# Kernel optimization log

Measured on AMD Instinct MI355X. Metric: run time of the kernel, lower is better.

The kernel has to match this reference:

```python
import jax, jax.numpy as jnp
import numpy as np

N_HEADS = 8
DIM_HEAD = 64


def _lin_params(key, fan_in, fan_out):
    k1, k2 = jax.random.split(key)
    w = jax.random.normal(k1, (fan_out, fan_in), jnp.float32) * 0.02
    b = jax.random.normal(k2, (fan_out,), jnp.float32) * 0.02
    return w, b


def setup_inputs() -> dict:
    key = jax.random.key(0)
    ks = jax.random.split(key, 16)
    n_nodes, n_edges = 30000, 480000
    input_nf, output_nf, hidden_nf = 128, 128, 256
    hd = N_HEADS * DIM_HEAD
    inp = {}
    inp['h'] = jax.random.normal(ks[0], (n_nodes, input_nf), jnp.float32)
    inp['x'] = jax.random.normal(ks[1], (n_nodes, 3), jnp.float32)
    inp['edge_index'] = jax.random.randint(ks[2], (2, n_edges), 0, n_nodes, jnp.int64)
    inp['mask'] = jnp.ones((n_edges,), jnp.bool_)
    inp['wq'], inp['bq'] = _lin_params(ks[3], input_nf, hd)
    inp['wk'], inp['bk'] = _lin_params(ks[4], input_nf, hd)
    inp['wv'], inp['bv'] = _lin_params(ks[5], input_nf, hd)
    inp['wo'], inp['bo'] = _lin_params(ks[6], hd, output_nf)
    inp['pw1'], inp['pb1'] = _lin_params(ks[7], 6, hidden_nf)
    inp['pw2'], inp['pb2'] = _lin_params(ks[8], hidden_nf, N_HEADS)
    inp['ew1'], inp['eb1'] = _lin_params(ks[9], 2 * input_nf + 7, hidden_nf)
    inp['ew2'], inp['eb2'] = _lin_params(ks[10], hidden_nf, hidden_nf)
    inp['eww'], inp['ewb'] = _lin_params(ks[11], hidden_nf, N_HEADS)
    inp['cw1'], inp['cb1'] = _lin_params(ks[12], 3, hidden_nf)
    inp['cw2'], inp['cb2'] = _lin_params(ks[13], hidden_nf, hidden_nf)
    inp['cw3'], inp['cb3'] = _lin_params(ks[14], hidden_nf, output_nf)
    return inp


def reference(h, x, edge_index, mask,
              wq, bq, wk, bk, wv, bv, wo, bo,
              pw1, pb1, pw2, pb2,
              ew1, eb1, ew2, eb2, eww, ewb,
              cw1, cb1, cw2, cb2, cw3, cb3):
    n_nodes = h.shape[0]
    row, col = edge_index[0], edge_index[1]
    # node projections -> [n, H, D]
    q = (h @ wq.T + bq).reshape(n_nodes, N_HEADS, DIM_HEAD)
    k = (h @ wk.T + bk).reshape(n_nodes, N_HEADS, DIM_HEAD)
    v = (h @ wv.T + bv).reshape(n_nodes, N_HEADS, DIM_HEAD)
    xr, xc = x[row], x[col]
    # pos encoding [E, H]
    abs_pos = jnp.concatenate([xr, xc], axis=-1)
    pos_enc = jax.nn.silu(abs_pos @ pw1.T + pb1) @ pw2.T + pb2
    # edge features -> per-head edge weights [E, H]
    rel_dist = jnp.sum((xr - xc) ** 2, axis=-1, keepdims=True)
    edge_attr = jnp.concatenate([h[row], h[col], rel_dist, xr, xc], axis=-1)
    edge_feat = jax.nn.silu(edge_attr @ ew1.T + eb1) @ ew2.T + eb2
    edge_w = edge_feat @ eww.T + ewb
    # attention scores [E, H]
    score = jnp.einsum('ehd,ehd->eh', q[row], k[col]) / (DIM_HEAD ** 0.5)
    score = score + pos_enc + edge_w
    score = jnp.where(mask[:, None], score, jnp.float32(-1e9))
    # scatter-softmax over edges grouped by destination (row)
    smax = jax.ops.segment_max(score, row, num_segments=n_nodes)
    escore = jnp.exp(score - smax[row])
    ssum = jax.ops.segment_sum(escore, row, num_segments=n_nodes)
    attn = escore / (ssum[row] + 1e-8)
    # weighted aggregation [n, H, D]
    agg = jax.ops.segment_sum(attn[:, :, None] * v[col], row, num_segments=n_nodes)
    out = agg.reshape(n_nodes, -1) @ wo.T + bo
    coord = jax.nn.silu(x @ cw1.T + cb1)
    coord = jax.nn.silu(coord @ cw2.T + cb2)
    coord = coord @ cw3.T + cb3
    return out + coord, jnp.zeros_like(x)
```

## Files before the change

kernel.cpp:

```cpp
#include <hip/hip_runtime.h>

typedef unsigned int uint;
typedef unsigned short ushort;
typedef unsigned char uchar;
typedef __attribute__((ext_vector_type(8))) short bf16x8;
typedef __attribute__((ext_vector_type(8))) ushort ushort8;
typedef __attribute__((ext_vector_type(4))) float f32x4;

__device__ __forceinline__ float silu_f(float t) { return t / (1.f + expf(-t)); }
__device__ __forceinline__ float silu_fast(float t) { return t / (1.f + __expf(-t)); }

__device__ __forceinline__ float bf2f(ushort u) {
  union { uint i; float f; } v; v.i = ((uint)u) << 16; return v.f;
}
__device__ __forceinline__ ushort f2bf(float f) {
  union { float f; uint i; } v; v.f = f;
  uint r = (v.i + 0x7fffu + ((v.i >> 16) & 1u)) >> 16;
  return (ushort)r;
}
__device__ __forceinline__ uchar f2e4m3(float f) {
  uint u = __float_as_uint(f);
  uint s = (u >> 24) & 0x80u;
  uint m = u & 0x7fffffffu;
  if (m >= 0x43f00000u) return (uchar)(s | 0x7e);
  if (m >= 0x3c800000u) {
    uint r = m + 0x7ffffu + ((m >> 20) & 1u);
    uint e = (r >> 23) - 120u;
    if (e > 15u) return (uchar)(s | 0x7e);
    return (uchar)(s | (e << 3) | ((r >> 20) & 7u));
  }
  float az = __uint_as_float(m);
  uint k = (uint)__float2int_rn(az * 512.f);
  return (uchar)(s | k);
}
__device__ __forceinline__ float e4m3f(uint b) {
  uint u = ((b & 0x80u) << 24) | ((b & 0x7fu) << 20);
  return __uint_as_float(u) * 0x1p+120f;
}

__global__ __launch_bounds__(256) void h2bf_kernel(const float* __restrict__ h,
                                                   ushort* __restrict__ h_bf, int total) {
  int idx = blockIdx.x * 256 + threadIdx.x;
  if (idx * 4 >= total) return;
  float4 v = *(const float4*)(h + idx * 4);
  ushort4 o;
  o.x = f2bf(v.x); o.y = f2bf(v.y); o.z = f2bf(v.z); o.w = f2bf(v.w);
  *(ushort4*)(h_bf + idx * 4) = o;
}

__global__ __launch_bounds__(256) void prep_wqkv(const float* __restrict__ wq,
                                                 const float* __restrict__ wk,
                                                 const float* __restrict__ wv,
                                                 const float* __restrict__ bq,
                                                 const float* __restrict__ bk,
                                                 const float* __restrict__ bv,
                                                 ushort* __restrict__ wqkv,
                                                 float* __restrict__ bqkv) {
  int idx = blockIdx.x * 256 + threadIdx.x;
  if (idx >= 1536 * 128) return;
  int j = idx >> 7, k = idx & 127;
  float v = (j < 512) ? wq[j * 128 + k]
          : (j < 1024) ? wk[(j - 512) * 128 + k]
          : wv[(j - 1024) * 128 + k];
  wqkv[idx] = f2bf(v);
  if (idx < 1536)
    bqkv[idx] = (idx < 512) ? bq[idx] : (idx < 1024) ? bk[idx - 512] : bv[idx - 1024];
}

__global__ __launch_bounds__(256) void prep_w1t(const float* __restrict__ ew1,
                                                const float* __restrict__ eb1,
                                                const float* __restrict__ pw1,
                                                const float* __restrict__ pb1,
                                                short* __restrict__ W1T,
                                                float* __restrict__ b1big) {
  int idx = blockIdx.x * 256 + threadIdx.x;
  if (idx >= 512 * 288) return;
  int n = idx / 288, k = idx % 288;
  float v = 0.f;
  if (n < 256) { if (k < 263) v = ew1[n * 263 + k]; }
  else         { if (k >= 257 && k < 263) v = pw1[(n - 256) * 6 + (k - 257)]; }
  W1T[idx] = (short)f2bf(v);
  if (idx < 512) b1big[idx] = (idx < 256) ? eb1[idx] : pb1[idx - 256];
}

__global__ __launch_bounds__(256) void prep_w2t(const float* __restrict__ ew2,
                                                const float* __restrict__ eww,
                                                const float* __restrict__ eb2,
                                                const float* __restrict__ ewb,
                                                const float* __restrict__ pw2,
                                                const float* __restrict__ pb2,
                                                short* __restrict__ W2T,
                                                float* __restrict__ biasC) {
  int idx = blockIdx.x * 256 + threadIdx.x;
  if (idx >= 16 * 512) return;
  int hh = idx >> 9, k = idx & 511;
  float v = 0.f;
  if (hh < 8) {
    if (k < 256) {
      float s = 0.f;
      for (int j = 0; j < 256; ++j) s += eww[hh * 256 + j] * ew2[j * 256 + k];
      v = s;
    } else {
      v = pw2[hh * 256 + (k - 256)];
    }
  }
  W2T[idx] = (short)f2bf(v);
  if (idx < 16) {
    float b = 0.f;
    if (idx < 8) {
      float s = 0.f;
      for (int j = 0; j < 256; ++j) s += eww[idx * 256 + j] * eb2[j];
      b = s + ewb[idx] + pb2[idx];
    }
    biasC[idx] = b;
  }
}

__global__ __launch_bounds__(256) void prep_wcomb(const float* __restrict__ wo,
                                                  const float* __restrict__ cw3,
                                                  const float* __restrict__ bo,
                                                  const float* __restrict__ cb3,
                                                  ushort* __restrict__ wcomb,
                                                  float* __restrict__ bcomb) {
  int idx = blockIdx.x * 256 + threadIdx.x;
  if (idx >= 128 * 768) return;
  int j = idx / 768, k = idx % 768;
  float v = (k < 512) ? wo[j * 512 + k] : cw3[j * 256 + (k - 512)];
  wcomb[idx] = f2bf(v);
  if (idx < 128) bcomb[idx] = bo[idx] + cb3[idx];
}

__global__ __launch_bounds__(256) void prep_cw2bf(const float* __restrict__ cw2,
                                                  ushort* __restrict__ cw2bf) {
  int idx = blockIdx.x * 256 + threadIdx.x;
  if (idx >= 256 * 256) return;
  cw2bf[idx] = f2bf(cw2[idx]);
}

__global__ __launch_bounds__(256) void qkv_mfma_kernel(
    const ushort* __restrict__ h_bf,
    const ushort* __restrict__ wqkv,
    const float* __restrict__ bqkv,
    ushort* __restrict__ q_t, uchar* __restrict__ k8, ushort* __restrict__ v_t,
    int n)
{
  __shared__ float oS[64 * 68];
  int tid = threadIdx.x;
  int lane = tid & 63, w = tid >> 6;
  int l15 = lane & 15, l4 = lane >> 4;
  int m0 = blockIdx.x * 64;
  int jb = blockIdx.y;
  int n0 = jb * 64 + w * 16;

  f32x4 acc[4];
#pragma unroll
  for (int mf = 0; mf < 4; ++mf) acc[mf] = (f32x4){0.f, 0.f, 0.f, 0.f};

#pragma unroll
  for (int ks = 0; ks < 4; ++ks) {
    bf16x8 bW = *(const bf16x8*)(wqkv + (size_t)(n0 + l15) * 128 + ks * 32 + l4 * 8);
#pragma unroll
    for (int mf = 0; mf < 4; ++mf) {
      int gr = m0 + mf * 16 + l15; if (gr >= n) gr = n - 1;
      bf16x8 aH = *(const bf16x8*)(h_bf + (size_t)gr * 128 + ks * 32 + l4 * 8);
      acc[mf] = __builtin_amdgcn_mfma_f32_16x16x32_bf16(aH, bW, acc[mf], 0, 0, 0);
    }
  }
#pragma unroll
  for (int mf = 0; mf < 4; ++mf)
#pragma unroll
    for (int i = 0; i < 4; ++i)
      oS[(mf * 16 + l4 * 4 + i) * 68 + w * 16 + l15] = acc[mf][i];
  __syncthreads();
  {
    int row = tid >> 2, cs = (tid & 3) * 16;
    int gr = m0 + row;
    if (gr < n) {
      int gc = jb * 64 + cs;
      int tbl = gc >> 9, cc = gc & 511;
      if (tbl == 1) {
        uint w0 = 0, w1 = 0, w2 = 0, w3 = 0;
#pragma unroll
        for (int j = 0; j < 4; ++j) w0 |= ((uint)f2e4m3(oS[row * 68 + cs + j] + bqkv[gc + j])) << (8 * j);
#pragma unroll
        for (int j = 0; j < 4; ++j) w1 |= ((uint)f2e4m3(oS[row * 68 + cs + 4 + j] + bqkv[gc + 4 + j])) << (8 * j);
#pragma unroll
        for (int j = 0; j < 4; ++j) w2 |= ((uint)f2e4m3(oS[row * 68 + cs + 8 + j] + bqkv[gc + 8 + j])) << (8 * j);
#pragma unroll
        for (int j = 0; j < 4; ++j) w3 |= ((uint)f2e4m3(oS[row * 68 + cs + 12 + j] + bqkv[gc + 12 + j])) << (8 * j);
        uint4 st = {w0, w1, w2, w3};
        *(uint4*)(k8 + (size_t)gr * 512 + cc) = st;
      } else {
        ushort* base = (tbl == 0) ? q_t : v_t;
        ushort8 o0, o1;
#pragma unroll
        for (int j = 0; j < 8; ++j) o0[j] = f2bf(oS[row * 68 + cs + j] + bqkv[gc + j]);
#pragma unroll
        for (int j = 0; j < 8; ++j) o1[j] = f2bf(oS[row * 68 + cs + 8 + j] + bqkv[gc + 8 + j]);
        *(ushort8*)(base + (size_t)gr * 512 + cc) = o0;
        *(ushort8*)(base + (size_t)gr * 512 + cc + 8) = o1;
      }
    }
  }
}

#define EB 64
#define AS 296
#define TS 72

__global__ __launch_bounds__(256, 2) void edge_mfma_kernel(
    const ushort* __restrict__ h_bf, const float* __restrict__ x,
    const int* __restrict__ ei, int E,
    const short* __restrict__ W1T, const float* __restrict__ b1big,
    const short* __restrict__ W2T, const float* __restrict__ biasC,
    float* __restrict__ scores)
{
  extern __shared__ char smem[];
  short* Albuf = (short*)smem;
  short* T1    = Albuf + EB * AS;
  float* slab  = (float*)smem;

  int tid = threadIdx.x;
  int lane = tid & 63, w = tid >> 6;
  int l15 = lane & 15, l4 = lane >> 4;
  int eb0 = blockIdx.x * EB;

  {
    int e = tid >> 2, p = tid & 3;
    int eg = eb0 + e; if (eg >= E) eg = E - 1;
    int r = ei[eg], c = ei[E + eg];
    const ushort* hr = h_bf + (size_t)r * 128 + p * 32;
    const ushort* hc = h_bf + (size_t)c * 128 + p * 32;
    short* arow = Albuf + e * AS;
#pragma unroll
    for (int i = 0; i < 4; ++i)
      *(uint4*)(arow + p * 32 + i * 8) = *(const uint4*)(hr + i * 8);
#pragma unroll
    for (int i = 0; i < 4; ++i)
      *(uint4*)(arow + 128 + p * 32 + i * 8) = *(const uint4*)(hc + i * 8);
    if (p == 0) {
      float xr0 = x[r*3], xr1 = x[r*3+1], xr2 = x[r*3+2];
      float xc0 = x[c*3], xc1 = x[c*3+1], xc2 = x[c*3+2];
      float d0 = xr0-xc0, d1 = xr1-xc1, d2 = xr2-xc2;
      bf16x8 g;
      g[0] = (short)f2bf(d0*d0 + d1*d1 + d2*d2);
      g[1] = (short)f2bf(xr0); g[2] = (short)f2bf(xr1); g[3] = (short)f2bf(xr2);
      g[4] = (short)f2bf(xc0); g[5] = (short)f2bf(xc1); g[6] = (short)f2bf(xc2);
      g[7] = 0;
      *(bf16x8*)(arow + 256) = g;
    } else {
      bf16x8 z = {0,0,0,0,0,0,0,0};
      *(bf16x8*)(arow + 256 + p * 8) = z;
    }
  }
  __syncthreads();

  f32x4 sacc[4];
#pragma unroll
  for (int ef = 0; ef < 4; ++ef) sacc[ef] = (f32x4){0.f, 0.f, 0.f, 0.f};

  short* t1w = T1 + w * (EB * TS);

#pragma unroll
  for (int cch = 0; cch < 2; ++cch) {
    const int n0 = cch ? (256 + w * 64) : (w * 64);
    const int ks0 = cch ? 8 : 0;
    f32x4 acc[4][4];
#pragma unroll
    for (int mf = 0; mf < 4; ++mf)
#pragma unroll
      for (int ef = 0; ef < 4; ++ef) acc[mf][ef] = (f32x4){0.f, 0.f, 0.f, 0.f};

    for (int ks = ks0; ks < 9; ++ks) {
      bf16x8 aW[4], bE[4];
#pragma unroll
      for (int mf = 0; mf < 4; ++mf)
        aW[mf] = *(const bf16x8*)(W1T + (size_t)(n0 + mf * 16 + l15) * 288 + ks * 32 + l4 * 8);
#pragma unroll
      for (int ef = 0; ef < 4; ++ef)
        bE[ef] = *(const bf16x8*)(Albuf + (ef * 16 + l15) * AS + ks * 32 + l4 * 8);
#pragma unroll
      for (int mf = 0; mf < 4; ++mf)
#pragma unroll
        for (int ef = 0; ef < 4; ++ef)
          acc[mf][ef] = __builtin_amdgcn_mfma_f32_16x16x32_bf16(aW[mf], bE[ef], acc[mf][ef], 0, 0, 0);
    }
#pragma unroll
    for (int mf = 0; mf < 4; ++mf) {
      int nl = mf * 16 + l4 * 4;
      float4 bias = *(const float4*)(b1big + n0 + nl);
#pragma unroll
      for (int ef = 0; ef < 4; ++ef) {
        int e = ef * 16 + l15;
        f32x4 v = acc[mf][ef];
        float s0 = silu_fast(v[0] + bias.x);
        float s1 = silu_fast(v[1] + bias.y);
        float s2 = silu_fast(v[2] + bias.z);
        float s3 = silu_fast(v[3] + bias.w);
        uint2 pk;
        asm("v_cvt_pk_bf16_f32 %0, %1, %2" : "=v"(pk.x) : "v"(s0), "v"(s1));
        asm("v_cvt_pk_bf16_f32 %0, %1, %2" : "=v"(pk.y) : "v"(s2), "v"(s3));
        *(uint2*)(t1w + e * TS + nl) = pk;
      }
    }
#pragma unroll
    for (int ks2 = 0; ks2 < 2; ++ks2) {
      bf16x8 bW2 = *(const bf16x8*)(W2T + (size_t)l15 * 512 + n0 + ks2 * 32 + l4 * 8);
#pragma unroll
      for (int ef = 0; ef < 4; ++ef) {
        bf16x8 aT = *(const bf16x8*)(t1w + (ef * 16 + l15) * TS + ks2 * 32 + l4 * 8);
        sacc[ef] = __builtin_amdgcn_mfma_f32_16x16x32_bf16(aT, bW2, sacc[ef], 0, 0, 0);
      }
    }
  }
  __syncthreads();
#pragma unroll
  for (int ef = 0; ef < 4; ++ef)
#pragma unroll
    for (int i = 0; i < 4; ++i)
      slab[(w * EB + ef * 16 + l4 * 4 + i) * 16 + l15] = sacc[ef][i];
  __syncthreads();
  for (int t = tid; t < EB * 8; t += 256) {
    int e = t >> 3, hh = t & 7;
    float s = biasC[hh]
            + slab[(0 * EB + e) * 16 + hh] + slab[(1 * EB + e) * 16 + hh]
            + slab[(2 * EB + e) * 16 + hh] + slab[(3 * EB + e) * 16 + hh];
    if (eb0 + e < E) scores[(size_t)(eb0 + e) * 8 + hh] = s;
  }
}

__global__ __launch_bounds__(256) void count_kernel(const int* __restrict__ ei,
                                                    int* __restrict__ cnt, int E) {
  int e = blockIdx.x * 256 + threadIdx.x;
  if (e < E) atomicAdd(&cnt[ei[e]], 1);
}

__global__ __launch_bounds__(1024) void scan_kernel(int* __restrict__ cnt,
                                                    int* __restrict__ offs, int n) {
  __shared__ int part[1024];
  int t = threadIdx.x;
  int chunk = (n + 1023) >> 10;
  int s = t * chunk, e = min(s + chunk, n);
  int sum = 0;
  for (int i = s; i < e; ++i) sum += cnt[i];
  part[t] = sum;
  __syncthreads();
  for (int off = 1; off < 1024; off <<= 1) {
    int v = (t >= off) ? part[t - off] : 0;
    __syncthreads();
    part[t] += v;
    __syncthreads();
  }
  int run = (t == 0) ? 0 : part[t - 1];
  for (int i = s; i < e; ++i) {
    int c = cnt[i];
    offs[i] = run;
    cnt[i] = run;
    run += c;
  }
  if (t == 1023) offs[n] = run;
}

__global__ __launch_bounds__(256) void fill_kernel(const int* __restrict__ ei,
                                                   int* __restrict__ cursor,
                                                   int2* __restrict__ pairs, int E) {
  int e = blockIdx.x * 256 + threadIdx.x;
  if (e < E) {
    int p = atomicAdd(&cursor[ei[e]], 1);
    pairs[p] = make_int2(e, ei[E + e]);
  }
}

__global__ __launch_bounds__(256) void attn_fused_kernel(
    const int* __restrict__ offs,
    const int2* __restrict__ pairs,
    const int* __restrict__ mask,
    const float* __restrict__ scores,
    const ushort* __restrict__ q_t,
    const uchar* __restrict__ k8,
    const ushort* __restrict__ v_t,
    ushort* __restrict__ agg, int n)
{
  int node = blockIdx.x * 4 + (threadIdx.x >> 6);
  if (node >= n) return;
  int lane = threadIdx.x & 63;
  int start = offs[node], end = offs[node + 1];

  bf16x8 qv = *(const bf16x8*)(q_t + (size_t)node * 512 + lane * 8);
  float qf[8];
#pragma unroll
  for (int j = 0; j < 8; ++j) qf[j] = bf2f((ushort)qv[j]);

  float m = -3.0e38f, ssum = 0.f;
  float acc[8];
#pragma unroll
  for (int j = 0; j < 8; ++j) acc[j] = 0.f;

  for (int i = start; i < end; ++i) {
    int2 pr = pairs[i];
    int eid = pr.x, col = pr.y;
    uint2 kw = *(const uint2*)(k8 + (size_t)col * 512 + lane * 8);
    bf16x8 vv = *(const bf16x8*)(v_t + (size_t)col * 512 + lane * 8);
    float dot = 0.f;
#pragma unroll
    for (int j = 0; j < 4; ++j)
      dot = fmaf(qf[j], e4m3f((kw.x >> (8 * j)) & 0xffu), dot);
#pragma unroll
    for (int j = 0; j < 4; ++j)
      dot = fmaf(qf[4 + j], e4m3f((kw.y >> (8 * j)) & 0xffu), dot);
    dot += __shfl_xor(dot, 1);
    dot += __shfl_xor(dot, 2);
    dot += __shfl_xor(dot, 4);
    float sml = scores[(size_t)eid * 8 + (lane >> 3)];
    float s = mask[eid] ? fmaf(dot, 0.125f, sml) : -1e9f;
    if (s > m) {
      float scale = __expf(m - s);
      ssum *= scale;
#pragma unroll
      for (int j = 0; j < 8; ++j) acc[j] *= scale;
      m = s;
    }
    float e = __expf(s - m);
    ssum += e;
#pragma unroll
    for (int j = 0; j < 8; ++j) acc[j] = fmaf(e, bf2f((ushort)vv[j]), acc[j]);
  }
  float inv = 1.f / (ssum + 1e-8f);
  ushort8 ov;
#pragma unroll
  for (int j = 0; j < 8; ++j) ov[j] = f2bf(acc[j] * inv);
  *(ushort8*)(agg + (size_t)node * 512 + lane * 8) = ov;
}

__global__ __launch_bounds__(256) void coord_c1_kernel(const float* __restrict__ x,
                                                       const float* __restrict__ cw1,
                                                       const float* __restrict__ cb1,
                                                       ushort* __restrict__ c1, int n) {
  int idx = blockIdx.x * 256 + threadIdx.x;
  if (idx >= n * 256) return;
  int node = idx >> 8, j = idx & 255;
  float t = fmaf(x[node * 3 + 2], cw1[j * 3 + 2],
            fmaf(x[node * 3 + 1], cw1[j * 3 + 1],
            fmaf(x[node * 3 + 0], cw1[j * 3 + 0], cb1[j])));
  c1[idx] = f2bf(silu_fast(t));
}

__global__ __launch_bounds__(256) void c2_mfma_kernel(const ushort* __restrict__ c1,
                                                      const ushort* __restrict__ cw2bf,
                                                      const float* __restrict__ cb2,
                                                      ushort* __restrict__ c2, int n) {
  __shared__ float oS[64 * 68];
  int tid = threadIdx.x;
  int lane = tid & 63, w = tid >> 6;
  int l15 = lane & 15, l4 = lane >> 4;
  int m0 = blockIdx.x * 64;
  int n0 = blockIdx.y * 64 + w * 16;

  f32x4 acc[4];
#pragma unroll
  for (int mf = 0; mf < 4; ++mf) acc[mf] = (f32x4){0.f, 0.f, 0.f, 0.f};
#pragma unroll
  for (int ks = 0; ks < 8; ++ks) {
    bf16x8 bW = *(const bf16x8*)(cw2bf + (size_t)(n0 + l15) * 256 + ks * 32 + l4 * 8);
#pragma unroll
    for (int mf = 0; mf < 4; ++mf) {
      int gr = m0 + mf * 16 + l15; if (gr >= n) gr = n - 1;
      bf16x8 aH = *(const bf16x8*)(c1 + (size_t)gr * 256 + ks * 32 + l4 * 8);
      acc[mf] = __builtin_amdgcn_mfma_f32_16x16x32_bf16(aH, bW, acc[mf], 0, 0, 0);
    }
  }
#pragma unroll
  for (int mf = 0; mf < 4; ++mf)
#pragma unroll
    for (int i = 0; i < 4; ++i)
      oS[(mf * 16 + l4 * 4 + i) * 68 + w * 16 + l15] = acc[mf][i];
  __syncthreads();
  {
    int row = tid >> 2, cs = (tid & 3) * 16;
    int gr = m0 + row;
    if (gr < n) {
      int gc = blockIdx.y * 64 + cs;
      ushort8 o0, o1;
#pragma unroll
      for (int j = 0; j < 8; ++j) o0[j] = f2bf(silu_fast(oS[row * 68 + cs + j] + cb2[gc + j]));
#pragma unroll
      for (int j = 0; j < 8; ++j) o1[j] = f2bf(silu_fast(oS[row * 68 + cs + 8 + j] + cb2[gc + 8 + j]));
      *(ushort8*)(c2 + (size_t)gr * 256 + gc) = o0;
      *(ushort8*)(c2 + (size_t)gr * 256 + gc + 8) = o1;
    }
  }
}

__global__ __launch_bounds__(256) void final_mfma_kernel(const ushort* __restrict__ agg,
                                                         const ushort* __restrict__ c2,
                                                         const ushort* __restrict__ wcomb,
                                                         const float* __restrict__ bcomb,
                                                         float* __restrict__ out, int n) {
  __shared__ float oS[64 * 68];
  int tid = threadIdx.x;
  int lane = tid & 63, w = tid >> 6;
  int l15 = lane & 15, l4 = lane >> 4;
  int m0 = blockIdx.x * 64;
  int jb = blockIdx.y;
  int n0 = jb * 64 + w * 16;

  f32x4 acc[4];
#pragma unroll
  for (int mf = 0; mf < 4; ++mf) acc[mf] = (f32x4){0.f, 0.f, 0.f, 0.f};
#pragma unroll
  for (int ks = 0; ks < 24; ++ks) {
    bf16x8 bW = *(const bf16x8*)(wcomb + (size_t)(n0 + l15) * 768 + ks * 32 + l4 * 8);
#pragma unroll
    for (int mf = 0; mf < 4; ++mf) {
      int gr = m0 + mf * 16 + l15; if (gr >= n) gr = n - 1;
      const ushort* ap = (ks < 16) ? (agg + (size_t)gr * 512 + ks * 32)
                                   : (c2 + (size_t)gr * 256 + (ks - 16) * 32);
      bf16x8 aH = *(const bf16x8*)(ap + l4 * 8);
      acc[mf] = __builtin_amdgcn_mfma_f32_16x16x32_bf16(aH, bW, acc[mf], 0, 0, 0);
    }
  }
#pragma unroll
  for (int mf = 0; mf < 4; ++mf)
#pragma unroll
    for (int i = 0; i < 4; ++i)
      oS[(mf * 16 + l4 * 4 + i) * 68 + w * 16 + l15] = acc[mf][i];
  __syncthreads();
  {
    int row = tid >> 2, cs = (tid & 3) * 16;
    int gr = m0 + row;
    if (gr < n) {
      int gc = jb * 64 + cs;
#pragma unroll
      for (int g = 0; g < 4; ++g) {
        float4 o;
        o.x = oS[row * 68 + cs + g * 4 + 0] + bcomb[gc + g * 4 + 0];
        o.y = oS[row * 68 + cs + g * 4 + 1] + bcomb[gc + g * 4 + 1];
        o.z = oS[row * 68 + cs + g * 4 + 2] + bcomb[gc + g * 4 + 2];
        o.w = oS[row * 68 + cs + g * 4 + 3] + bcomb[gc + g * 4 + 3];
        *(float4*)(out + (size_t)gr * 128 + gc + g * 4) = o;
      }
    }
  }
}

extern "C" void kernel_launch(void* const* d_in, const int* in_sizes, int n_in,
                              void* d_out, int out_size, void* d_ws, size_t ws_size,
                              hipStream_t stream) {
  const float* h   = (const float*)d_in[0];
  const float* x   = (const float*)d_in[1];
  const int*   ei  = (const int*)d_in[2];
  const int*   mask= (const int*)d_in[3];
  const float* wq  = (const float*)d_in[4];
  const float* bq  = (const float*)d_in[5];
  const float* wk  = (const float*)d_in[6];
  const float* bk  = (const float*)d_in[7];
  const float* wv  = (const float*)d_in[8];
  const float* bv  = (const float*)d_in[9];
  const float* wo  = (const float*)d_in[10];
  const float* bo  = (const float*)d_in[11];
  const float* pw1 = (const float*)d_in[12];
  const float* pb1 = (const float*)d_in[13];
  const float* pw2 = (const float*)d_in[14];
  const float* pb2 = (const float*)d_in[15];
  const float* ew1 = (const float*)d_in[16];
  const float* eb1 = (const float*)d_in[17];
  const float* ew2 = (const float*)d_in[18];
  const float* eb2 = (const float*)d_in[19];
  const float* eww = (const float*)d_in[20];
  const float* ewb = (const float*)d_in[21];
  const float* cw1 = (const float*)d_in[22];
  const float* cb1 = (const float*)d_in[23];
  const float* cw2 = (const float*)d_in[24];
  const float* cb2 = (const float*)d_in[25];
  const float* cw3 = (const float*)d_in[26];
  const float* cb3 = (const float*)d_in[27];

  int n = in_sizes[0] / 128;
  int E = in_sizes[3];

  char* wptr = (char*)d_ws;
  auto alloc = [&](size_t bytes) {
    char* p = wptr;
    wptr += (bytes + 255) & ~(size_t)255;
    return p;
  };
  ushort* q_t   = (ushort*)alloc((size_t)n * 512 * 2);
  uchar*  k8    = (uchar*)alloc((size_t)n * 512);
  ushort* v_t   = (ushort*)alloc((size_t)n * 512 * 2);
  ushort* h_bf  = (ushort*)alloc((size_t)n * 128 * 2);
  float* scores = (float*)alloc((size_t)E * 8 * 4);
  ushort* agg   = (ushort*)alloc((size_t)n * 512 * 2);
  ushort* c1    = (ushort*)alloc((size_t)n * 256 * 2);
  ushort* c2    = (ushort*)alloc((size_t)n * 256 * 2);
  ushort* wqkv  = (ushort*)alloc((size_t)1536 * 128 * 2);
  float* bqkv   = (float*)alloc((size_t)1536 * 4);
  short* W1T    = (short*)alloc((size_t)512 * 288 * 2);
  float* b1big  = (float*)alloc((size_t)512 * 4);
  short* W2T    = (short*)alloc((size_t)16 * 512 * 2);
  float* biasC  = (float*)alloc((size_t)16 * 4);
  ushort* wcomb = (ushort*)alloc((size_t)128 * 768 * 2);
  float* bcomb  = (float*)alloc((size_t)128 * 4);
  ushort* cw2bf = (ushort*)alloc((size_t)256 * 256 * 2);
  int* offs     = (int*)alloc((size_t)(n + 1) * 4);
  int* cursor   = (int*)alloc((size_t)n * 4);
  int2* pairs   = (int2*)alloc((size_t)E * 8);

  hipMemsetAsync(cursor, 0, (size_t)n * 4, stream);

  h2bf_kernel<<<dim3((n * 128 / 4 + 255) / 256), 256, 0, stream>>>(h, h_bf, n * 128);
  prep_wqkv<<<dim3((1536 * 128 + 255) / 256), 256, 0, stream>>>(wq, wk, wv, bq, bk, bv, wqkv, bqkv);
  prep_w1t<<<dim3((512 * 288 + 255) / 256), 256, 0, stream>>>(ew1, eb1, pw1, pb1, W1T, b1big);
  prep_w2t<<<dim3((16 * 512 + 255) / 256), 256, 0, stream>>>(ew2, eww, eb2, ewb, pw2, pb2, W2T, biasC);
  prep_wcomb<<<dim3((128 * 768 + 255) / 256), 256, 0, stream>>>(wo, cw3, bo, cb3, wcomb, bcomb);
  prep_cw2bf<<<dim3((256 * 256 + 255) / 256), 256, 0, stream>>>(cw2, cw2bf);

  qkv_mfma_kernel<<<dim3((n + 63) / 64, 24), 256, 0, stream>>>(h_bf, wqkv, bqkv, q_t, k8, v_t, n);

  size_t edge_lds = (size_t)(EB * AS + 4 * EB * TS) * 2;
  edge_mfma_kernel<<<dim3((E + EB - 1) / EB), 256, edge_lds, stream>>>(
      h_bf, x, ei, E, W1T, b1big, W2T, biasC, scores);

  count_kernel<<<dim3((E + 255) / 256), 256, 0, stream>>>(ei, cursor, E);
  scan_kernel<<<dim3(1), 1024, 0, stream>>>(cursor, offs, n);
  fill_kernel<<<dim3((E + 255) / 256), 256, 0, stream>>>(ei, cursor, pairs, E);

  attn_fused_kernel<<<dim3((n + 3) / 4), 256, 0, stream>>>(
      offs, pairs, mask, scores, q_t, k8, v_t, agg, n);

  coord_c1_kernel<<<dim3((n * 256 + 255) / 256), 256, 0, stream>>>(x, cw1, cb1, c1, n);
  c2_mfma_kernel<<<dim3((n + 63) / 64, 4), 256, 0, stream>>>(c1, cw2bf, cb2, c2, n);

  hipMemsetAsync((float*)d_out + (size_t)n * 128, 0, (size_t)n * 3 * 4, stream);
  final_mfma_kernel<<<dim3((n + 63) / 64, 2), 256, 0, stream>>>(agg, c2, wcomb, bcomb,
                                                                (float*)d_out, n);
}
```

Before: 711.0 us.

## Merge prep kernels, restructure QKV and edge GEMMs, pipeline attention loop

Merges the weight-prep, h-to-bf16, coord layer-1 and edge-count kernels into one launch that picks its work by block-index range. The QKV GEMM now runs one block per 64 rows that loops over all output tiles, keeping the h fragments in registers and storing straight from the accumulators without an LDS staging pass. The edge kernel no longer stages h rows in LDS; it reads them from global memory per k-step, which shrinks LDS and raises the occupancy hint from 2 to 4. The attention loop prefetches the next edge's K/V/score and replaces the branchy online-softmax update with a branchless one. SiLU now uses a hardware reciprocal. The changes cut launch overhead and LDS traffic, but the edge GEMM now issues repeated uncoalesced global gathers.

```diff
diff --git a/kernel.cpp b/kernel.cpp
--- a/kernel.cpp
+++ b/kernel.cpp
@@ -7,9 +7,9 @@
 typedef __attribute__((ext_vector_type(8))) ushort ushort8;
 typedef __attribute__((ext_vector_type(4))) float f32x4;
 
-__device__ __forceinline__ float silu_f(float t) { return t / (1.f + expf(-t)); }
-__device__ __forceinline__ float silu_fast(float t) { return t / (1.f + __expf(-t)); }
-
+__device__ __forceinline__ float silu_fast(float t) {
+  return t * __builtin_amdgcn_rcpf(1.f + __expf(-t));
+}
 __device__ __forceinline__ float bf2f(ushort u) {
   union { uint i; float f; } v; v.i = ((uint)u) << 16; return v.f;
 }
@@ -38,222 +38,210 @@
   return __uint_as_float(u) * 0x1p+120f;
 }
 
-__global__ __launch_bounds__(256) void h2bf_kernel(const float* __restrict__ h,
-                                                   ushort* __restrict__ h_bf, int total) {
-  int idx = blockIdx.x * 256 + threadIdx.x;
-  if (idx * 4 >= total) return;
-  float4 v = *(const float4*)(h + idx * 4);
-  ushort4 o;
-  o.x = f2bf(v.x); o.y = f2bf(v.y); o.z = f2bf(v.z); o.w = f2bf(v.w);
-  *(ushort4*)(h_bf + idx * 4) = o;
-}
-
-__global__ __launch_bounds__(256) void prep_wqkv(const float* __restrict__ wq,
-                                                 const float* __restrict__ wk,
-                                                 const float* __restrict__ wv,
-                                                 const float* __restrict__ bq,
-                                                 const float* __restrict__ bk,
-                                                 const float* __restrict__ bv,
-                                                 ushort* __restrict__ wqkv,
-                                                 float* __restrict__ bqkv) {
-  int idx = blockIdx.x * 256 + threadIdx.x;
-  if (idx >= 1536 * 128) return;
-  int j = idx >> 7, k = idx & 127;
-  float v = (j < 512) ? wq[j * 128 + k]
-          : (j < 1024) ? wk[(j - 512) * 128 + k]
-          : wv[(j - 1024) * 128 + k];
-  wqkv[idx] = f2bf(v);
-  if (idx < 1536)
-    bqkv[idx] = (idx < 512) ? bq[idx] : (idx < 1024) ? bk[idx - 512] : bv[idx - 1024];
-}
-
-__global__ __launch_bounds__(256) void prep_w1t(const float* __restrict__ ew1,
-                                                const float* __restrict__ eb1,
-                                                const float* __restrict__ pw1,
-                                                const float* __restrict__ pb1,
-                                                short* __restrict__ W1T,
-                                                float* __restrict__ b1big) {
-  int idx = blockIdx.x * 256 + threadIdx.x;
-  if (idx >= 512 * 288) return;
-  int n = idx / 288, k = idx % 288;
-  float v = 0.f;
-  if (n < 256) { if (k < 263) v = ew1[n * 263 + k]; }
-  else         { if (k >= 257 && k < 263) v = pw1[(n - 256) * 6 + (k - 257)]; }
-  W1T[idx] = (short)f2bf(v);
-  if (idx < 512) b1big[idx] = (idx < 256) ? eb1[idx] : pb1[idx - 256];
-}
-
-__global__ __launch_bounds__(256) void prep_w2t(const float* __restrict__ ew2,
-                                                const float* __restrict__ eww,
-                                                const float* __restrict__ eb2,
-                                                const float* __restrict__ ewb,
-                                                const float* __restrict__ pw2,
-                                                const float* __restrict__ pb2,
-                                                short* __restrict__ W2T,
-                                                float* __restrict__ biasC) {
-  int idx = blockIdx.x * 256 + threadIdx.x;
-  if (idx >= 16 * 512) return;
-  int hh = idx >> 9, k = idx & 511;
-  float v = 0.f;
-  if (hh < 8) {
-    if (k < 256) {
-      float s = 0.f;
-      for (int j = 0; j < 256; ++j) s += eww[hh * 256 + j] * ew2[j * 256 + k];
-      v = s;
-    } else {
-      v = pw2[hh * 256 + (k - 256)];
-    }
-  }
-  W2T[idx] = (short)f2bf(v);
-  if (idx < 16) {
-    float b = 0.f;
-    if (idx < 8) {
-      float s = 0.f;
-      for (int j = 0; j < 256; ++j) s += eww[idx * 256 + j] * eb2[j];
-      b = s + ewb[idx] + pb2[idx];
-    }
-    biasC[idx] = b;
-  }
-}
-
-__global__ __launch_bounds__(256) void prep_wcomb(const float* __restrict__ wo,
-                                                  const float* __restrict__ cw3,
-                                                  const float* __restrict__ bo,
-                                                  const float* __restrict__ cb3,
-                                                  ushort* __restrict__ wcomb,
-                                                  float* __restrict__ bcomb) {
-  int idx = blockIdx.x * 256 + threadIdx.x;
-  if (idx >= 128 * 768) return;
-  int j = idx / 768, k = idx % 768;
-  float v = (k < 512) ? wo[j * 512 + k] : cw3[j * 256 + (k - 512)];
-  wcomb[idx] = f2bf(v);
-  if (idx < 128) bcomb[idx] = bo[idx] + cb3[idx];
-}
-
-__global__ __launch_bounds__(256) void prep_cw2bf(const float* __restrict__ cw2,
-                                                  ushort* __restrict__ cw2bf) {
-  int idx = blockIdx.x * 256 + threadIdx.x;
-  if (idx >= 256 * 256) return;
-  cw2bf[idx] = f2bf(cw2[idx]);
-}
-
-__global__ __launch_bounds__(256) void qkv_mfma_kernel(
+__global__ __launch_bounds__(256) void mega_prep(
+    const float* __restrict__ h, const float* __restrict__ x,
+    const int* __restrict__ ei,
+    const float* __restrict__ wq, const float* __restrict__ wk, const float* __restrict__ wv,
+    const float* __restrict__ bq, const float* __restrict__ bk, const float* __restrict__ bv,
+    const float* __restrict__ ew1, const float* __restrict__ eb1,
+    const float* __restrict__ pw1, const float* __restrict__ pb1,
+    const float* __restrict__ ew2, const float* __restrict__ eww,
+    const float* __restrict__ eb2, const float* __restrict__ ewb,
+    const float* __restrict__ pw2, const float* __restrict__ pb2,
+    const float* __restrict__ wo, const float* __restrict__ cw3,
+    const float* __restrict__ bo, const float* __restrict__ cb3,
+    const float* __restrict__ cw1, const float* __restrict__ cb1,
+    const float* __restrict__ cw2,
+    ushort* __restrict__ h_bf, ushort* __restrict__ c1,
+    ushort* __restrict__ wqkv, float* __restrict__ bqkv,
+    short* __restrict__ W1T, float* __restrict__ b1big,
+    short* __restrict__ W2T, float* __restrict__ biasC,
+    ushort* __restrict__ wcomb, float* __restrict__ bcomb,
+    ushort* __restrict__ cw2bf, int* __restrict__ cnt,
+    int n, int E,
+    int o1, int o2, int o3, int o4, int o5, int o6, int o7)
+{
+  int b = blockIdx.x, tid = threadIdx.x;
+  if (b < o1) {
+    int idx = b * 256 + tid;
+    if (idx * 4 < n * 128) {
+      float4 v = *(const float4*)(h + idx * 4);
+      ushort4 o; o.x = f2bf(v.x); o.y = f2bf(v.y); o.z = f2bf(v.z); o.w = f2bf(v.w);
+      *(ushort4*)(h_bf + idx * 4) = o;
+    }
+  } else if (b < o2) {
+    int idx = (b - o1) * 256 + tid;
+    if (idx < n * 256) {
+      int node = idx >> 8, j = idx & 255;
+      float t = fmaf(x[node * 3 + 2], cw1[j * 3 + 2],
+                fmaf(x[node * 3 + 1], cw1[j * 3 + 1],
+                fmaf(x[node * 3 + 0], cw1[j * 3 + 0], cb1[j])));
+      c1[idx] = f2bf(silu_fast(t));
+    }
+  } else if (b < o3) {
+    int idx = (b - o2) * 256 + tid;
+    if (idx < 1536 * 128) {
+      int j = idx >> 7, k = idx & 127;
+      float v = (j < 512) ? wq[j * 128 + k]
+              : (j < 1024) ? wk[(j - 512) * 128 + k]
+              : wv[(j - 1024) * 128 + k];
+      wqkv[idx] = f2bf(v);
+      if (idx < 1536)
+        bqkv[idx] = (idx < 512) ? bq[idx] : (idx < 1024) ? bk[idx - 512] : bv[idx - 1024];
+    }
+  } else if (b < o4) {
+    int idx = (b - o3) * 256 + tid;
+    if (idx < 512 * 288) {
+      int nn = idx / 288, k = idx % 288;
+      float v = 0.f;
+      if (nn < 256) { if (k < 263) v = ew1[nn * 263 + k]; }
+      else          { if (k >= 257 && k < 263) v = pw1[(nn - 256) * 6 + (k - 257)]; }
+      W1T[idx] = (short)f2bf(v);
+      if (idx < 512) b1big[idx] = (idx < 256) ? eb1[idx] : pb1[idx - 256];
+    }
+  } else if (b < o5) {
+    int idx = (b - o4) * 256 + tid;
+    if (idx < 16 * 512) {
+      int hh = idx >> 9, k = idx & 511;
+      float v = 0.f;
+      if (hh < 8) {
+        if (k < 256) {
+          float s = 0.f;
+          for (int j = 0; j < 256; ++j) s += eww[hh * 256 + j] * ew2[j * 256 + k];
+          v = s;
+        } else v = pw2[hh * 256 + (k - 256)];
+      }
+      W2T[idx] = (short)f2bf(v);
+      if (idx < 16) {
+        float bb = 0.f;
+        if (idx < 8) {
+          float s = 0.f;
+          for (int j = 0; j < 256; ++j) s += eww[idx * 256 + j] * eb2[j];
+          bb = s + ewb[idx] + pb2[idx];
+        }
+        biasC[idx] = bb;
+      }
+    }
+  } else if (b < o6) {
+    int idx = (b - o5) * 256 + tid;
+    if (idx < 128 * 768) {
+      int j = idx / 768, k = idx % 768;
+      float v = (k < 512) ? wo[j * 512 + k] : cw3[j * 256 + (k - 512)];
+      wcomb[idx] = f2bf(v);
+      if (idx < 128) bcomb[idx] = bo[idx] + cb3[idx];
+    }
+  } else if (b < o7) {
+    int idx = (b - o6) * 256 + tid;
+    if (idx < 256 * 256) cw2bf[idx] = f2bf(cw2[idx]);
+  } else {
+    int e = (b - o7) * 256 + tid;
+    if (e < E) atomicAdd(&cnt[ei[e]], 1);
+  }
+}
+
+__global__ __launch_bounds__(256) void qkv_mfma2_kernel(
     const ushort* __restrict__ h_bf,
     const ushort* __restrict__ wqkv,
     const float* __restrict__ bqkv,
     ushort* __restrict__ q_t, uchar* __restrict__ k8, ushort* __restrict__ v_t,
     int n)
 {
-  __shared__ float oS[64 * 68];
   int tid = threadIdx.x;
   int lane = tid & 63, w = tid >> 6;
   int l15 = lane & 15, l4 = lane >> 4;
   int m0 = blockIdx.x * 64;
-  int jb = blockIdx.y;
-  int n0 = jb * 64 + w * 16;
-
-  f32x4 acc[4];
-#pragma unroll
-  for (int mf = 0; mf < 4; ++mf) acc[mf] = (f32x4){0.f, 0.f, 0.f, 0.f};
-
-#pragma unroll
-  for (int ks = 0; ks < 4; ++ks) {
-    bf16x8 bW = *(const bf16x8*)(wqkv + (size_t)(n0 + l15) * 128 + ks * 32 + l4 * 8);
-#pragma unroll
-    for (int mf = 0; mf < 4; ++mf) {
-      int gr = m0 + mf * 16 + l15; if (gr >= n) gr = n - 1;
-      bf16x8 aH = *(const bf16x8*)(h_bf + (size_t)gr * 128 + ks * 32 + l4 * 8);
-      acc[mf] = __builtin_amdgcn_mfma_f32_16x16x32_bf16(aH, bW, acc[mf], 0, 0, 0);
-    }
-  }
-#pragma unroll
-  for (int mf = 0; mf < 4; ++mf)
-#pragma unroll
-    for (int i = 0; i < 4; ++i)
-      oS[(mf * 16 + l4 * 4 + i) * 68 + w * 16 + l15] = acc[mf][i];
-  __syncthreads();
-  {
-    int row = tid >> 2, cs = (tid & 3) * 16;
-    int gr = m0 + row;
-    if (gr < n) {
-      int gc = jb * 64 + cs;
-      int tbl = gc >> 9, cc = gc & 511;
-      if (tbl == 1) {
-        uint w0 = 0, w1 = 0, w2 = 0, w3 = 0;
-#pragma unroll
-        for (int j = 0; j < 4; ++j) w0 |= ((uint)f2e4m3(oS[row * 68 + cs + j] + bqkv[gc + j])) << (8 * j);
-#pragma unroll
-        for (int j = 0; j < 4; ++j) w1 |= ((uint)f2e4m3(oS[row * 68 + cs + 4 + j] + bqkv[gc + 4 + j])) << (8 * j);
-#pragma unroll
-        for (int j = 0; j < 4; ++j) w2 |= ((uint)f2e4m3(oS[row * 68 + cs + 8 + j] + bqkv[gc + 8 + j])) << (8 * j);
-#pragma unroll
-        for (int j = 0; j < 4; ++j) w3 |= ((uint)f2e4m3(oS[row * 68 + cs + 12 + j] + bqkv[gc + 12 + j])) << (8 * j);
-        uint4 st = {w0, w1, w2, w3};
-        *(uint4*)(k8 + (size_t)gr * 512 + cc) = st;
-      } else {
-        ushort* base = (tbl == 0) ? q_t : v_t;
-        ushort8 o0, o1;
-#pragma unroll
-        for (int j = 0; j < 8; ++j) o0[j] = f2bf(oS[row * 68 + cs + j] + bqkv[gc + j]);
-#pragma unroll
-        for (int j = 0; j < 8; ++j) o1[j] = f2bf(oS[row * 68 + cs + 8 + j] + bqkv[gc + 8 + j]);
-        *(ushort8*)(base + (size_t)gr * 512 + cc) = o0;
-        *(ushort8*)(base + (size_t)gr * 512 + cc + 8) = o1;
+  int mrow = m0 + w * 16 + l15;
+  bool valid = mrow < n;
+  int mr = valid ? mrow : (n - 1);
+
+  bf16x8 hf[4];
+#pragma unroll
+  for (int ks = 0; ks < 4; ++ks)
+    hf[ks] = *(const bf16x8*)(h_bf + (size_t)mr * 128 + ks * 32 + l4 * 8);
+
+  for (int jb = 0; jb < 24; ++jb) {
+    f32x4 acc[4];
+#pragma unroll
+    for (int nf = 0; nf < 4; ++nf) acc[nf] = (f32x4){0.f, 0.f, 0.f, 0.f};
+#pragma unroll
+    for (int nf = 0; nf < 4; ++nf)
+#pragma unroll
+      for (int ks = 0; ks < 4; ++ks) {
+        bf16x8 wf = *(const bf16x8*)(wqkv + (size_t)(jb * 64 + nf * 16 + l15) * 128 + ks * 32 + l4 * 8);
+        acc[nf] = __builtin_amdgcn_mfma_f32_16x16x32_bf16(wf, hf[ks], acc[nf], 0, 0, 0);
+      }
+    if (valid) {
+#pragma unroll
+      for (int nf = 0; nf < 4; ++nf) {
+        int gc = jb * 64 + nf * 16 + l4 * 4;
+        float4 bb = *(const float4*)(bqkv + gc);
+        float v0 = acc[nf][0] + bb.x, v1 = acc[nf][1] + bb.y;
+        float v2 = acc[nf][2] + bb.z, v3 = acc[nf][3] + bb.w;
+        if (jb < 8) {
+          ushort4 st; st.x = f2bf(v0); st.y = f2bf(v1); st.z = f2bf(v2); st.w = f2bf(v3);
+          *(ushort4*)(q_t + (size_t)mrow * 512 + gc) = st;
+        } else if (jb < 16) {
+          uint pk = (uint)f2e4m3(v0) | ((uint)f2e4m3(v1) << 8)
+                  | ((uint)f2e4m3(v2) << 16) | ((uint)f2e4m3(v3) << 24);
+          *(uint*)(k8 + (size_t)mrow * 512 + (gc - 512)) = pk;
+        } else {
+          ushort4 st; st.x = f2bf(v0); st.y = f2bf(v1); st.z = f2bf(v2); st.w = f2bf(v3);
+          *(ushort4*)(v_t + (size_t)mrow * 512 + (gc - 1024)) = st;
+        }
       }
     }
   }
 }
 
 #define EB 64
-#define AS 296
+#define GS 32
 #define TS 72
 
-__global__ __launch_bounds__(256, 2) void edge_mfma_kernel(
+__global__ __launch_bounds__(256, 4) void edge_mfma2_kernel(
     const ushort* __restrict__ h_bf, const float* __restrict__ x,
     const int* __restrict__ ei, int E,
     const short* __restrict__ W1T, const float* __restrict__ b1big,
     const short* __restrict__ W2T, const float* __restrict__ biasC,
     float* __restrict__ scores)
 {
-  extern __shared__ char smem[];
-  short* Albuf = (short*)smem;
-  short* T1    = Albuf + EB * AS;
-  float* slab  = (float*)smem;
+  __shared__ short geomL[EB * GS];
+  __shared__ short T1[4 * EB * TS];
+  float* slab = (float*)T1;
 
   int tid = threadIdx.x;
   int lane = tid & 63, w = tid >> 6;
   int l15 = lane & 15, l4 = lane >> 4;
   int eb0 = blockIdx.x * EB;
 
-  {
-    int e = tid >> 2, p = tid & 3;
-    int eg = eb0 + e; if (eg >= E) eg = E - 1;
+  if (tid < EB) {
+    int eg = min(eb0 + tid, E - 1);
     int r = ei[eg], c = ei[E + eg];
-    const ushort* hr = h_bf + (size_t)r * 128 + p * 32;
-    const ushort* hc = h_bf + (size_t)c * 128 + p * 32;
-    short* arow = Albuf + e * AS;
-#pragma unroll
-    for (int i = 0; i < 4; ++i)
-      *(uint4*)(arow + p * 32 + i * 8) = *(const uint4*)(hr + i * 8);
-#pragma unroll
-    for (int i = 0; i < 4; ++i)
-      *(uint4*)(arow + 128 + p * 32 + i * 8) = *(const uint4*)(hc + i * 8);
-    if (p == 0) {
-      float xr0 = x[r*3], xr1 = x[r*3+1], xr2 = x[r*3+2];
-      float xc0 = x[c*3], xc1 = x[c*3+1], xc2 = x[c*3+2];
-      float d0 = xr0-xc0, d1 = xr1-xc1, d2 = xr2-xc2;
-      bf16x8 g;
-      g[0] = (short)f2bf(d0*d0 + d1*d1 + d2*d2);
-      g[1] = (short)f2bf(xr0); g[2] = (short)f2bf(xr1); g[3] = (short)f2bf(xr2);
-      g[4] = (short)f2bf(xc0); g[5] = (short)f2bf(xc1); g[6] = (short)f2bf(xc2);
-      g[7] = 0;
-      *(bf16x8*)(arow + 256) = g;
-    } else {
-      bf16x8 z = {0,0,0,0,0,0,0,0};
-      *(bf16x8*)(arow + 256 + p * 8) = z;
-    }
+    float xr0 = x[r*3], xr1 = x[r*3+1], xr2 = x[r*3+2];
+    float xc0 = x[c*3], xc1 = x[c*3+1], xc2 = x[c*3+2];
+    float d0 = xr0-xc0, d1 = xr1-xc1, d2 = xr2-xc2;
+    bf16x8 g;
+    g[0] = (short)f2bf(d0*d0 + d1*d1 + d2*d2);
+    g[1] = (short)f2bf(xr0); g[2] = (short)f2bf(xr1); g[3] = (short)f2bf(xr2);
+    g[4] = (short)f2bf(xc0); g[5] = (short)f2bf(xc1); g[6] = (short)f2bf(xc2);
+    g[7] = 0;
+    bf16x8 z = {0,0,0,0,0,0,0,0};
+    *(bf16x8*)(geomL + tid * GS) = g;
+    *(bf16x8*)(geomL + tid * GS + 8) = z;
+    *(bf16x8*)(geomL + tid * GS + 16) = z;
+    *(bf16x8*)(geomL + tid * GS + 24) = z;
   }
   __syncthreads();
+
+  const char* hb = (const char*)h_bf;
+  uint ro[4], co[4], ga[4];
+#pragma unroll
+  for (int ef = 0; ef < 4; ++ef) {
+    int eg = min(eb0 + ef * 16 + l15, E - 1);
+    int r = ei[eg], c = ei[E + eg];
+    ro[ef] = (uint)r * 256 + l4 * 16;
+    co[ef] = (uint)c * 256 + l4 * 16;
+    ga[ef] = (uint)(ef * 16 + l15) * (GS * 2) + l4 * 16;
+  }
 
   f32x4 sacc[4];
 #pragma unroll
@@ -271,14 +259,18 @@
 #pragma unroll
       for (int ef = 0; ef < 4; ++ef) acc[mf][ef] = (f32x4){0.f, 0.f, 0.f, 0.f};
 
+#pragma unroll
     for (int ks = ks0; ks < 9; ++ks) {
       bf16x8 aW[4], bE[4];
 #pragma unroll
       for (int mf = 0; mf < 4; ++mf)
         aW[mf] = *(const bf16x8*)(W1T + (size_t)(n0 + mf * 16 + l15) * 288 + ks * 32 + l4 * 8);
 #pragma unroll
-      for (int ef = 0; ef < 4; ++ef)
-        bE[ef] = *(const bf16x8*)(Albuf + (ef * 16 + l15) * AS + ks * 32 + l4 * 8);
+      for (int ef = 0; ef < 4; ++ef) {
+        if (ks < 4)      bE[ef] = *(const bf16x8*)(hb + ro[ef] + ks * 64);
+        else if (ks < 8) bE[ef] = *(const bf16x8*)(hb + co[ef] + (ks - 4) * 64);
+        else             bE[ef] = *(const bf16x8*)((const char*)geomL + ga[ef]);
+      }
 #pragma unroll
       for (int mf = 0; mf < 4; ++mf)
 #pragma unroll
@@ -327,12 +319,6 @@
             + slab[(2 * EB + e) * 16 + hh] + slab[(3 * EB + e) * 16 + hh];
     if (eb0 + e < E) scores[(size_t)(eb0 + e) * 8 + hh] = s;
   }
-}
-
-__global__ __launch_bounds__(256) void count_kernel(const int* __restrict__ ei,
-                                                    int* __restrict__ cnt, int E) {
-  int e = blockIdx.x * 256 + threadIdx.x;
-  if (e < E) atomicAdd(&cnt[ei[e]], 1);
 }
 
 __global__ __launch_bounds__(1024) void scan_kernel(int* __restrict__ cnt,
@@ -396,53 +382,48 @@
 #pragma unroll
   for (int j = 0; j < 8; ++j) acc[j] = 0.f;
 
-  for (int i = start; i < end; ++i) {
-    int2 pr = pairs[i];
-    int eid = pr.x, col = pr.y;
-    uint2 kw = *(const uint2*)(k8 + (size_t)col * 512 + lane * 8);
-    bf16x8 vv = *(const bf16x8*)(v_t + (size_t)col * 512 + lane * 8);
-    float dot = 0.f;
-#pragma unroll
-    for (int j = 0; j < 4; ++j)
-      dot = fmaf(qf[j], e4m3f((kw.x >> (8 * j)) & 0xffu), dot);
-#pragma unroll
-    for (int j = 0; j < 4; ++j)
-      dot = fmaf(qf[4 + j], e4m3f((kw.y >> (8 * j)) & 0xffu), dot);
-    dot += __shfl_xor(dot, 1);
-    dot += __shfl_xor(dot, 2);
-    dot += __shfl_xor(dot, 4);
-    float sml = scores[(size_t)eid * 8 + (lane >> 3)];
-    float s = mask[eid] ? fmaf(dot, 0.125f, sml) : -1e9f;
-    if (s > m) {
-      float scale = __expf(m - s);
-      ssum *= scale;
-#pragma unroll
-      for (int j = 0; j < 8; ++j) acc[j] *= scale;
-      m = s;
-    }
-    float e = __expf(s - m);
-    ssum += e;
-#pragma unroll
-    for (int j = 0; j < 8; ++j) acc[j] = fmaf(e, bf2f((ushort)vv[j]), acc[j]);
-  }
-  float inv = 1.f / (ssum + 1e-8f);
+  if (start < end) {
+    int2 pr = pairs[start];
+    uint2 kw = *(const uint2*)(k8 + (size_t)pr.y * 512 + lane * 8);
+    bf16x8 vv = *(const bf16x8*)(v_t + (size_t)pr.y * 512 + lane * 8);
+    float sml = scores[(size_t)pr.x * 8 + (lane >> 3)];
+    int mk = mask[pr.x];
+
+    for (int i = start; i < end; ++i) {
+      uint2 kwc = kw; bf16x8 vvc = vv; float smlc = sml; int mkc = mk;
+      int inx = (i + 1 < end) ? (i + 1) : i;
+      pr = pairs[inx];
+      kw = *(const uint2*)(k8 + (size_t)pr.y * 512 + lane * 8);
+      vv = *(const bf16x8*)(v_t + (size_t)pr.y * 512 + lane * 8);
+      sml = scores[(size_t)pr.x * 8 + (lane >> 3)];
+      mk = mask[pr.x];
+
+      float dot = 0.f;
+#pragma unroll
+      for (int j = 0; j < 4; ++j)
+        dot = fmaf(qf[j], e4m3f((kwc.x >> (8 * j)) & 0xffu), dot);
+#pragma unroll
+      for (int j = 0; j < 4; ++j)
+        dot = fmaf(qf[4 + j], e4m3f((kwc.y >> (8 * j)) & 0xffu), dot);
+      dot += __shfl_xor(dot, 1);
+      dot += __shfl_xor(dot, 2);
+      dot += __shfl_xor(dot, 4);
+      float s = mkc ? fmaf(dot, 0.125f, smlc) : -1e9f;
+      float nm = fmaxf(m, s);
+      float cs = __expf(m - nm);
+      float e  = __expf(s - nm);
+      ssum = fmaf(ssum, cs, e);
+#pragma unroll
+      for (int j = 0; j < 8; ++j)
+        acc[j] = fmaf(acc[j], cs, e * bf2f((ushort)vvc[j]));
+      m = nm;
+    }
+  }
+  float inv = __builtin_amdgcn_rcpf(ssum + 1e-8f);
   ushort8 ov;
 #pragma unroll
   for (int j = 0; j < 8; ++j) ov[j] = f2bf(acc[j] * inv);
   *(ushort8*)(agg + (size_t)node * 512 + lane * 8) = ov;
-}
-
-__global__ __launch_bounds__(256) void coord_c1_kernel(const float* __restrict__ x,
-                                                       const float* __restrict__ cw1,
-                                                       const float* __restrict__ cb1,
-                                                       ushort* __restrict__ c1, int n) {
-  int idx = blockIdx.x * 256 + threadIdx.x;
-  if (idx >= n * 256) return;
-  int node = idx >> 8, j = idx & 255;
-  float t = fmaf(x[node * 3 + 2], cw1[j * 3 + 2],
-            fmaf(x[node * 3 + 1], cw1[j * 3 + 1],
-            fmaf(x[node * 3 + 0], cw1[j * 3 + 0], cb1[j])));
-  c1[idx] = f2bf(silu_fast(t));
 }
 
 __global__ __launch_bounds__(256) void c2_mfma_kernel(const ushort* __restrict__ c1,
@@ -607,27 +588,35 @@
 
   hipMemsetAsync(cursor, 0, (size_t)n * 4, stream);
 
-  h2bf_kernel<<<dim3((n * 128 / 4 + 255) / 256), 256, 0, stream>>>(h, h_bf, n * 128);
-  prep_wqkv<<<dim3((1536 * 128 + 255) / 256), 256, 0, stream>>>(wq, wk, wv, bq, bk, bv, wqkv, bqkv);
-  prep_w1t<<<dim3((512 * 288 + 255) / 256), 256, 0, stream>>>(ew1, eb1, pw1, pb1, W1T, b1big);
-  prep_w2t<<<dim3((16 * 512 + 255) / 256), 256, 0, stream>>>(ew2, eww, eb2, ewb, pw2, pb2, W2T, biasC);
-  prep_wcomb<<<dim3((128 * 768 + 255) / 256), 256, 0, stream>>>(wo, cw3, bo, cb3, wcomb, bcomb);
-  prep_cw2bf<<<dim3((256 * 256 + 255) / 256), 256, 0, stream>>>(cw2, cw2bf);
-
-  qkv_mfma_kernel<<<dim3((n + 63) / 64, 24), 256, 0, stream>>>(h_bf, wqkv, bqkv, q_t, k8, v_t, n);
-
-  size_t edge_lds = (size_t)(EB * AS + 4 * EB * TS) * 2;
-  edge_mfma_kernel<<<dim3((E + EB - 1) / EB), 256, edge_lds, stream>>>(
-      h_bf, x, ei, E, W1T, b1big, W2T, biasC, scores);
-
-  count_kernel<<<dim3((E + 255) / 256), 256, 0, stream>>>(ei, cursor, E);
+  int b_h2  = (n * 128 / 4 + 255) / 256;
+  int b_c1  = (n * 256 + 255) / 256;
+  int b_wq  = (1536 * 128 + 255) / 256;
+  int b_w1  = (512 * 288 + 255) / 256;
+  int b_w2  = (16 * 512 + 255) / 256;
+  int b_wc  = (128 * 768 + 255) / 256;
+  int b_cw  = (256 * 256 + 255) / 256;
+  int b_cnt = (E + 255) / 256;
+  int o1 = b_h2, o2 = o1 + b_c1, o3 = o2 + b_wq, o4 = o3 + b_w1;
+  int o5 = o4 + b_w2, o6 = o5 + b_wc, o7 = o6 + b_cw;
+  int total_blocks = o7 + b_cnt;
+
+  mega_prep<<<dim3(total_blocks), 256, 0, stream>>>(
+      h, x, ei, wq, wk, wv, bq, bk, bv, ew1, eb1, pw1, pb1, ew2, eww, eb2, ewb,
+      pw2, pb2, wo, cw3, bo, cb3, cw1, cb1, cw2,
+      h_bf, c1, wqkv, bqkv, W1T, b1big, W2T, biasC, wcomb, bcomb, cw2bf, cursor,
+      n, E, o1, o2, o3, o4, o5, o6, o7);
+
   scan_kernel<<<dim3(1), 1024, 0, stream>>>(cursor, offs, n);
   fill_kernel<<<dim3((E + 255) / 256), 256, 0, stream>>>(ei, cursor, pairs, E);
 
+  qkv_mfma2_kernel<<<dim3((n + 63) / 64), 256, 0, stream>>>(h_bf, wqkv, bqkv, q_t, k8, v_t, n);
+
+  edge_mfma2_kernel<<<dim3((E + EB - 1) / EB), 256, 0, stream>>>(
+      h_bf, x, ei, E, W1T, b1big, W2T, biasC, scores);
+
   attn_fused_kernel<<<dim3((n + 3) / 4), 256, 0, stream>>>(
       offs, pairs, mask, scores, q_t, k8, v_t, agg, n);
 
-  coord_c1_kernel<<<dim3((n * 256 + 255) / 256), 256, 0, stream>>>(x, cw1, cb1, c1, n);
   c2_mfma_kernel<<<dim3((n + 63) / 64, 4), 256, 0, stream>>>(c1, cw2bf, cb2, c2, n);
 
   hipMemsetAsync((float*)d_out + (size_t)n * 128, 0, (size_t)n * 3 * 4, stream);
```

Result: no change. 701.0 us (-1.4%).
